# Kernel optimization log

Hardware: AMD Instinct MI355X
Metric: run time of the kernel (lower is better)

The kernel has to match this reference:

```python
import jax, jax.numpy as jnp
from jax import lax
import numpy as np

B, T = 4096, 32
VOCAB, E, H, NCLS = 10000, 300, 300, 2


def setup_inputs() -> dict:
    key = jax.random.key(0)
    ks = jax.random.split(key, 10)
    cap = jax.random.randint(ks[0], (B, T), 0, VOCAB)
    cap_len = jax.random.randint(ks[1], (B,), 1, T + 1)  # lengths in [1, T]
    embed_w = jax.random.uniform(ks[2], (VOCAB, E), jnp.float32, -0.1, 0.1)
    s = 1.0 / np.sqrt(H)
    W_ih = jax.random.uniform(ks[3], (4 * H, E), jnp.float32, -s, s)
    W_hh = jax.random.uniform(ks[4], (4 * H, H), jnp.float32, -s, s)
    b_ih = jax.random.uniform(ks[5], (4 * H,), jnp.float32, -s, s)
    b_hh = jax.random.uniform(ks[6], (4 * H,), jnp.float32, -s, s)
    cls_v = jax.random.normal(ks[7], (NCLS, H), jnp.float32) * 0.05
    cls_g = jnp.linalg.norm(cls_v, axis=1, keepdims=True)  # weight_norm init: g = ||v||
    cls_b = jax.random.uniform(ks[8], (NCLS,), jnp.float32, -s, s)
    return {"cap": cap, "cap_len": cap_len, "embed_w": embed_w,
            "W_ih": W_ih, "W_hh": W_hh, "b_ih": b_ih, "b_hh": b_hh,
            "cls_v": cls_v, "cls_g": cls_g, "cls_b": cls_b}


def _lstm_forward(cap, cap_len, embed_w, W_ih, W_hh, b_ih, b_hh, cls_v, cls_g, cls_b):
    bsz = cap.shape[0]
    hid = W_hh.shape[1]
    emb = embed_w[cap]                                   # [B, T, E]
    # Precompute the input projections for all timesteps at once (one big GEMM).
    x_gates = jnp.einsum('bte,ge->btg', emb, W_ih) + b_ih + b_hh  # [B, T, 4H]

    def step(carry, xg_t):
        h, c = carry
        gates = xg_t + h @ W_hh.T                        # [B, 4H]
        i, f, g, o = jnp.split(gates, 4, axis=-1)        # torch gate order i,f,g,o
        i = jax.nn.sigmoid(i)
        f = jax.nn.sigmoid(f)
        g = jnp.tanh(g)
        o = jax.nn.sigmoid(o)
        c = f * c + i * g
        h = o * jnp.tanh(c)
        return (h, c), h

    h0 = jnp.zeros((bsz, hid), emb.dtype)
    (_, _), hs = lax.scan(step, (h0, h0), jnp.swapaxes(x_gates, 0, 1))  # hs: [T, B, H]
    h_last = hs[cap_len - 1, jnp.arange(bsz)]            # last valid hidden state per sample
    # weight-normed classifier: W = g * v / ||v||_row  (dropout is identity in eval)
    W = cls_g * cls_v / jnp.linalg.norm(cls_v, axis=1, keepdims=True)
    return h_last @ W.T + cls_b


def reference(cap, cap_len, embed_w, W_ih, W_hh, b_ih, b_hh, cls_v, cls_g, cls_b):
    return _lstm_forward(cap, cap_len, embed_w, W_ih, W_hh, b_ih, b_hh, cls_v, cls_g, cls_b)
```

## Files before the change

kernel.cpp:

```cpp
#include <hip/hip_runtime.h>
#include <hip/hip_fp16.h>

typedef _Float16 f16;
typedef _Float16 f16x4 __attribute__((ext_vector_type(4)));
typedef _Float16 f16x8 __attribute__((ext_vector_type(8)));
typedef float f32x4 __attribute__((ext_vector_type(4)));

#define B_SZ   4096
#define T_SZ   32
#define VOCAB  10000
#define E_SZ   300
#define H_SZ   300
#define KP     320
#define GP     304
#define G4     1216
#define LDA    328
#define LDG    1224
#define LDC    308
#define ROWS   16
#define NBLK   (B_SZ/ROWS)

__device__ __forceinline__ float sigmoid_f(float x) {
    return 1.f / (1.f + __expf(-x));
}
__device__ __forceinline__ float tanh_f(float x) {
    return 2.f / (1.f + __expf(-2.f * x)) - 1.f;
}

__global__ void kP0(const float* __restrict__ ew, f16* __restrict__ embT) {
    int v = blockIdx.x, k = threadIdx.x;
    embT[(size_t)v * KP + k] = (k < E_SZ) ? (f16)ew[(size_t)v * E_SZ + k] : (f16)0.f;
}

__global__ void kPW2(const float* __restrict__ wih, const float* __restrict__ whh,
                     const float* __restrict__ bih, const float* __restrict__ bhh,
                     f16* __restrict__ Wpk, float* __restrict__ biasp) {
    int bid = blockIdx.x;
    int lane = threadIdx.x;
    int k = bid % 20, ntg = bid / 20;
    int nt = ntg % 19, gate = ntg / 19;
    int c = lane & 15, q = lane >> 4;
    int j = nt * 16 + c;
    int src = gate * H_SZ + j;
    f16 vals[8];
#pragma unroll
    for (int jj = 0; jj < 8; ++jj) {
        int kk = k * 32 + q * 8 + jj;
        float v = 0.f;
        if (j < H_SZ) {
            if (kk < KP) { if (kk < H_SZ) v = whh[(size_t)src * H_SZ + kk]; }
            else { int kx = kk - KP; if (kx < E_SZ) v = wih[(size_t)src * E_SZ + kx]; }
        }
        vals[jj] = (f16)v;
    }
    *(f16x8*)(Wpk + ((size_t)bid * 64 + lane) * 8) = *(const f16x8*)vals;
    if (k == 0 && q == 0)
        biasp[gate * GP + j] = (j < H_SZ) ? (bih[src] + bhh[src]) : 0.f;
}

__global__ void kPW4(const float* __restrict__ whh, f16* __restrict__ WgS) {
    int bid = blockIdx.x;
    int lane = threadIdx.x;
    int c = lane & 15, q = lane >> 4;
    f16 vals[8];
    if (bid < 760) {
        int nt = bid / 40, g = (bid % 40) / 10, k = bid % 10;
        int j = nt * 16 + c;
        int src = g * H_SZ + j;
#pragma unroll
        for (int jj = 0; jj < 8; ++jj) {
            int kk = k * 32 + q * 8 + jj;
            float v = (j < H_SZ && kk < H_SZ) ? whh[(size_t)src * H_SZ + kk] : 0.f;
            vals[jj] = (f16)v;
        }
    } else {
#pragma unroll
        for (int jj = 0; jj < 8; ++jj) vals[jj] = (f16)0.f;
    }
    *(f16x8*)(WgS + ((size_t)bid * 64 + lane) * 8) = *(const f16x8*)vals;
}

__global__ void kP2(const float* __restrict__ cls_v, const float* __restrict__ cls_g,
                    float* __restrict__ Wc) {
    int lane = threadIdx.x;
    for (int cl = 0; cl < 2; ++cl) {
        float s = 0.f;
        for (int j = lane; j < H_SZ; j += 64) { float v = cls_v[cl * H_SZ + j]; s += v * v; }
        for (int off = 32; off; off >>= 1) s += __shfl_down(s, off);
        float nrm = sqrtf(__shfl(s, 0));
        float scale = cls_g[cl] / nrm;
        for (int j = lane; j < GP; j += 64)
            Wc[cl * GP + j] = (j < H_SZ) ? cls_v[cl * H_SZ + j] * scale : 0.f;
    }
}

__global__ __launch_bounds__(512, 2)
void kX2(const f16* __restrict__ embT, const f16* __restrict__ Wpk,
         const float* __restrict__ biasp, f16* __restrict__ embX) {
    int tid = threadIdx.x;
    int v0 = blockIdx.x * 16;
    int wave = tid >> 6, lane = tid & 63;
    int c = lane & 15, q = lane >> 4;
    int gate = wave >> 1, half = wave & 1;
    int nt0 = half * 10, ntiles = half ? 9 : 10;
    const f16* wp0 = Wpk + (((size_t)(gate * 19 + nt0) * 20 + 10) * 64 + lane) * 8;
    f16x8 afr[10];
    const f16* arow = embT + (size_t)(v0 + c) * KP + q * 8;
#pragma unroll
    for (int k = 0; k < 10; ++k)
        afr[k] = *(const f16x8*)(arow + k * 32);
    f16x8 buf[10];
#pragma unroll
    for (int s = 0; s < 10; ++s)
        buf[s] = *(const f16x8*)(wp0 + (size_t)s * 512);
#pragma unroll 1
    for (int nt = 0; nt < ntiles - 1; ++nt) {
        int jcol = (nt0 + nt) * 16 + c;
        float bia = biasp[gate * GP + jcol];
        f32x4 acc = {bia, bia, bia, bia};
#pragma unroll
        for (int k = 0; k < 10; ++k) {
            acc = __builtin_amdgcn_mfma_f32_16x16x32_f16(afr[k], buf[k], acc, 0, 0, 0);
            buf[k] = *(const f16x8*)(wp0 + (size_t)(nt * 20 + k + 20) * 512);
        }
#pragma unroll
        for (int r = 0; r < 4; ++r)
            embX[((size_t)(v0 + q * 4 + r) * GP + jcol) * 4 + gate] = (f16)acc[r];
    }
    {
        int nt = ntiles - 1;
        int jcol = (nt0 + nt) * 16 + c;
        float bia = biasp[gate * GP + jcol];
        f32x4 acc = {bia, bia, bia, bia};
#pragma unroll
        for (int k = 0; k < 10; ++k)
            acc = __builtin_amdgcn_mfma_f32_16x16x32_f16(afr[k], buf[k], acc, 0, 0, 0);
#pragma unroll
        for (int r = 0; r < 4; ++r)
            embX[((size_t)(v0 + q * 4 + r) * GP + jcol) * 4 + gate] = (f16)acc[r];
    }
}

__global__ __launch_bounds__(512, 2)
void kR22(const int* __restrict__ cap,
          const int* __restrict__ cap_len,
          const f16* __restrict__ embX,
          const f16* __restrict__ WgS,
          const float* __restrict__ Wc,
          const float* __restrict__ cls_b,
          float* __restrict__ out) {
    extern __shared__ __align__(16) char smem[];
    f16*   hbufA = (f16*)smem;
    float* cbuf  = (float*)(smem + 20992);
    int*   capv  = (int*)(smem + 40704);
    int*   lens  = (int*)(smem + 42752);
    f16*   wres  = (f16*)(smem + 43008);
    int tid = threadIdx.x;
    int b0 = blockIdx.x * ROWS;
    if (tid < ROWS) lens[tid] = cap_len[b0 + tid];
    for (int i = tid; i < ROWS * T_SZ; i += 512) capv[i] = cap[(size_t)b0 * T_SZ + i];
    for (int i = tid; i < 2 * ROWS * LDA; i += 512) hbufA[i] = (f16)0.f;
    for (int i = tid; i < ROWS * LDC; i += 512) cbuf[i] = 0.f;

    int wave = tid >> 6, lane = tid & 63;
    int c = lane & 15, q = lane >> 4;
    int tstart = (wave < 5) ? 2 * wave : 10 + 3 * (wave - 5);
    int tcnt   = (wave < 5) ? 2 : 3;
    int Rw     = (wave < 5) ? 1 : 2;
    f16* resw = wres + ((wave < 5) ? wave * 5120 : 25600 + (wave - 5) * 10240);
    for (int u = 0; u < Rw; ++u)
#pragma unroll
        for (int k = 0; k < 10; ++k)
            *(f16x8*)(resw + (u * 10 + k) * 512 + lane * 8) =
                *(const f16x8*)(WgS + ((size_t)(tstart * 40 + u * 10 + k) * 64 + lane) * 8);
    __syncthreads();

    const f16* wp0 = WgS + ((size_t)(tstart * 40) * 64 + lane) * 8;
    int cur = 0;
    f16x8 buf[10];
#pragma unroll
    for (int s = 0; s < 10; ++s)
        buf[s] = *(const f16x8*)(wp0 + (size_t)(Rw * 10 + s) * 512);

    for (int t = 0; t < T_SZ; ++t) {
        const f16* hb = hbufA + cur * (ROWS * LDA);
        f16*       hn = hbufA + (cur ^ 1) * (ROWS * LDA);
        f16x8 afr[10];
#pragma unroll
        for (int k = 0; k < 10; ++k)
            afr[k] = *(const f16x8*)(hb + c * LDA + k * 32 + q * 8);
#pragma unroll 1
        for (int nt = 0; nt < tcnt; ++nt) {
            int col = (tstart + nt) * 16 + c;
            f16x4 xi[4];
#pragma unroll
            for (int r = 0; r < 4; ++r) {
                int v = capv[(q * 4 + r) * T_SZ + t];
                xi[r] = *(const f16x4*)(embX + (size_t)v * G4 + col * 4);
            }
            f32x4 acc0 = {0.f, 0.f, 0.f, 0.f};
            f32x4 acc1 = {0.f, 0.f, 0.f, 0.f};
            f32x4 acc2 = {0.f, 0.f, 0.f, 0.f};
            f32x4 acc3 = {0.f, 0.f, 0.f, 0.f};
#pragma unroll
            for (int g = 0; g < 4; ++g) {
                f32x4* ag = (g == 0) ? &acc0 : (g == 1) ? &acc1 : (g == 2) ? &acc2 : &acc3;
                if (nt == 0 && g < Rw) {
                    const f16* rb = resw + g * 5120 + lane * 8;
#pragma unroll
                    for (int k = 0; k < 10; ++k)
                        *ag = __builtin_amdgcn_mfma_f32_16x16x32_f16(
                            afr[k], *(const f16x8*)(rb + k * 512), *ag, 0, 0, 0);
                } else {
                    int nbase = (g < 3) ? (nt * 40 + (g + 1) * 10)
                              : ((nt + 1 < tcnt) ? (nt + 1) * 40 : Rw * 10);
#pragma unroll
                    for (int k = 0; k < 10; ++k) {
                        *ag = __builtin_amdgcn_mfma_f32_16x16x32_f16(
                            afr[k], buf[k], *ag, 0, 0, 0);
                        buf[k] = *(const f16x8*)(wp0 + (size_t)(nbase + k) * 512);
                    }
                }
            }
#pragma unroll
            for (int r = 0; r < 4; ++r) {
                int row = q * 4 + r;
                f16x4 xv = xi[r];
                float gi = acc0[r] + (float)xv[0];
                float gf = acc1[r] + (float)xv[1];
                float gg = acc2[r] + (float)xv[2];
                float go = acc3[r] + (float)xv[3];
                float ii = sigmoid_f(gi);
                float ff = sigmoid_f(gf);
                float gt = tanh_f(gg);
                float oo = sigmoid_f(go);
                int ci = row * LDC + col;
                float cn = ff * cbuf[ci] + ii * gt;
                cbuf[ci] = cn;
                float hh = oo * tanh_f(cn);
                hn[row * LDA + col] = (f16)hh;
                if (t == lens[row] - 1) {
                    float s0 = hh * Wc[col];
                    float s1 = hh * Wc[GP + col];
                    s0 += __shfl_xor(s0, 1); s1 += __shfl_xor(s1, 1);
                    s0 += __shfl_xor(s0, 2); s1 += __shfl_xor(s1, 2);
                    s0 += __shfl_xor(s0, 4); s1 += __shfl_xor(s1, 4);
                    s0 += __shfl_xor(s0, 8); s1 += __shfl_xor(s1, 8);
                    if (c == 0) {
                        if (wave == 0 && nt == 0) { s0 += cls_b[0]; s1 += cls_b[1]; }
                        atomicAdd(out + (size_t)(b0 + row) * 2 + 0, s0);
                        atomicAdd(out + (size_t)(b0 + row) * 2 + 1, s1);
                    }
                }
            }
        }
        __syncthreads();
        cur ^= 1;
    }
}

__global__ __launch_bounds__(512, 2)
void kR8(const int* __restrict__ cap,
         const int* __restrict__ cap_len,
         const f16* __restrict__ embT,
         const f16* __restrict__ Wpk,
         const float* __restrict__ biasp,
         float* __restrict__ hlast) {
    extern __shared__ __align__(16) char smem[];
    f16*   hbuf  = (f16*)smem;
    f16*   xbuf  = (f16*)(smem + 10496);
    f16*   gates = (f16*)(smem + 20992);
    float* biasL = (float*)(smem + 60160);
    int*   capv  = (int*)(smem + 65024);
    int*   lens  = (int*)(smem + 67072);
    int tid = threadIdx.x;
    int b0 = blockIdx.x * 16;
    if (tid < 16) lens[tid] = cap_len[b0 + tid];
    for (int i = tid; i < 16 * T_SZ; i += 512) capv[i] = cap[(size_t)b0 * T_SZ + i];
    for (int i = tid; i < 16 * LDA; i += 512) hbuf[i] = (f16)0.f;
    for (int i = tid; i < G4; i += 512) biasL[i] = biasp[i];
    __syncthreads();
    for (int i = tid; i < 16 * 40; i += 512) {
        int m = i / 40, c8 = i - m * 40;
        int v = capv[m * T_SZ + 0];
        *(f16x8*)(xbuf + m * LDA + c8 * 8) = *(const f16x8*)(embT + (size_t)v * KP + c8 * 8);
    }
    __syncthreads();
    int wave = tid >> 6, lane = tid & 63;
    int c = lane & 15, q = lane >> 4;
    int gate = wave >> 1, half = wave & 1;
    int nt0 = half * 10, ntiles = half ? 9 : 10;
    const f16* wp0 = Wpk + ((size_t)((gate * 19 + nt0) * 20) * 64 + lane) * 8;
    const f16* hrow = hbuf + c * LDA + q * 8;
    const f16* xrow = xbuf + c * LDA + q * 8;
    float creg[10];
#pragma unroll
    for (int i = 0; i < 10; ++i) creg[i] = 0.f;

    for (int t = 0; t < T_SZ; ++t) {
        f16x8 afr[10];
#pragma unroll
        for (int k = 0; k < 10; ++k)
            afr[k] = *(const f16x8*)(hrow + k * 32);
        f16x8 buf[10];
#pragma unroll
        for (int s = 0; s < 10; ++s)
            buf[s] = *(const f16x8*)(wp0 + (size_t)s * 512);
#pragma unroll 1
        for (int nt = 0; nt < ntiles - 1; ++nt) {
            int base = nt * 20;
            int ncol = gate * GP + (nt0 + nt) * 16 + c;
            float bia = biasL[ncol];
            f32x4 acch = {bia, bia, bia, bia};
            f32x4 accx = {0.f, 0.f, 0.f, 0.f};
#pragma unroll
            for (int k = 0; k < 20; ++k) {
                if (k < 10) {
                    acch = __builtin_amdgcn_mfma_f32_16x16x32_f16(afr[k], buf[k % 10], acch, 0, 0, 0);
                } else {
                    f16x8 a = *(const f16x8*)(xrow + (k - 10) * 32);
                    accx = __builtin_amdgcn_mfma_f32_16x16x32_f16(a, buf[k % 10], accx, 0, 0, 0);
                }
                buf[k % 10] = *(const f16x8*)(wp0 + (size_t)(base + k + 10) * 512);
            }
#pragma unroll
            for (int r = 0; r < 4; ++r)
                gates[(q * 4 + r) * LDG + ncol] = (f16)(acch[r] + accx[r]);
        }
        {
            int nt = ntiles - 1;
            int base = nt * 20;
            int ncol = gate * GP + (nt0 + nt) * 16 + c;
            float bia = biasL[ncol];
            f32x4 acch = {bia, bia, bia, bia};
            f32x4 accx = {0.f, 0.f, 0.f, 0.f};
#pragma unroll
            for (int k = 0; k < 20; ++k) {
                if (k < 10) {
                    acch = __builtin_amdgcn_mfma_f32_16x16x32_f16(afr[k], buf[k % 10], acch, 0, 0, 0);
                    buf[k % 10] = *(const f16x8*)(wp0 + (size_t)(base + k + 10) * 512);
                } else {
                    f16x8 a = *(const f16x8*)(xrow + (k - 10) * 32);
                    accx = __builtin_amdgcn_mfma_f32_16x16x32_f16(a, buf[k % 10], accx, 0, 0, 0);
                }
            }
#pragma unroll
            for (int r = 0; r < 4; ++r)
                gates[(q * 4 + r) * LDG + ncol] = (f16)(acch[r] + accx[r]);
        }
        __syncthreads();
        int tp1 = t + 1;
        if (tp1 < T_SZ) {
            for (int i = tid; i < 16 * 40; i += 512) {
                int m = i / 40, c8 = i - m * 40;
                int v = capv[m * T_SZ + tp1];
                *(f16x8*)(xbuf + m * LDA + c8 * 8) =
                    *(const f16x8*)(embT + (size_t)v * KP + c8 * 8);
            }
        }
#pragma unroll
        for (int it = 0; it < 10; ++it) {
            int idx = tid + it * 512;
            int m = idx / 320, j = idx - m * 320;
            if (j < H_SZ) {
                const f16* gr = gates + m * LDG;
                float gi = (float)gr[j];
                float gf = (float)gr[GP + j];
                float gg = (float)gr[2 * GP + j];
                float go = (float)gr[3 * GP + j];
                float ii = sigmoid_f(gi);
                float ff = sigmoid_f(gf);
                float gt = tanh_f(gg);
                float oo = sigmoid_f(go);
                float cn = ff * creg[it] + ii * gt;
                creg[it] = cn;
                float hh = oo * tanh_f(cn);
                hbuf[m * LDA + j] = (f16)hh;
                if (t == lens[m] - 1) hlast[(size_t)(b0 + m) * GP + j] = hh;
            }
        }
        __syncthreads();
    }
}

__global__ void kC(const float* __restrict__ hlast, const float* __restrict__ Wc,
                   const float* __restrict__ cls_b, float* __restrict__ out) {
    int row = blockIdx.x, lane = threadIdx.x;
    const float* h = hlast + (size_t)row * GP;
    float s0 = 0.f, s1 = 0.f;
    for (int j = lane; j < H_SZ; j += 64) {
        float hv = h[j];
        s0 += hv * Wc[j];
        s1 += hv * Wc[GP + j];
    }
    for (int off = 32; off; off >>= 1) {
        s0 += __shfl_down(s0, off);
        s1 += __shfl_down(s1, off);
    }
    if (lane == 0) {
        out[row * 2 + 0] = s0 + cls_b[0];
        out[row * 2 + 1] = s1 + cls_b[1];
    }
}

extern "C" void kernel_launch(void* const* d_in, const int* in_sizes, int n_in,
                              void* d_out, int out_size, void* d_ws, size_t ws_size,
                              hipStream_t stream) {
    const int*   cap     = (const int*)d_in[0];
    const int*   cap_len = (const int*)d_in[1];
    const float* embed_w = (const float*)d_in[2];
    const float* W_ih    = (const float*)d_in[3];
    const float* W_hh    = (const float*)d_in[4];
    const float* b_ih    = (const float*)d_in[5];
    const float* b_hh    = (const float*)d_in[6];
    const float* cls_v   = (const float*)d_in[7];
    const float* cls_g   = (const float*)d_in[8];
    const float* cls_b   = (const float*)d_in[9];
    float* out = (float*)d_out;

    char* w = (char*)d_ws;
    size_t off = 0;
    auto alloc = [&](size_t bytes) -> void* {
        void* p = w + off;
        off += (bytes + 255) & ~(size_t)255;
        return p;
    };
    f16*   embT  = (f16*)alloc((size_t)VOCAB * KP * sizeof(f16));
    f16*   Wpk   = (f16*)alloc((size_t)1520 * 64 * 8 * sizeof(f16));
    f16*   WgS   = (f16*)alloc((size_t)800 * 64 * 8 * sizeof(f16));
    float* biasp = (float*)alloc((size_t)G4 * sizeof(float));
    float* Wc    = (float*)alloc((size_t)2 * GP * sizeof(float));
    float* hlast = (float*)alloc((size_t)B_SZ * GP * sizeof(float));
    f16*   embX  = (f16*)(w + off);
    size_t need_split = off + ((size_t)VOCAB * GP * 4 * sizeof(f16) + 255);
    bool split = (ws_size >= need_split);

    kP0<<<VOCAB, KP, 0, stream>>>(embed_w, embT);
    kPW2<<<1520, 64, 0, stream>>>(W_ih, W_hh, b_ih, b_hh, Wpk, biasp);
    kP2<<<1, 64, 0, stream>>>(cls_v, cls_g, Wc);
    if (split) {
        (void)hipMemsetAsync(out, 0, (size_t)out_size, stream);
        kPW4<<<800, 64, 0, stream>>>(W_hh, WgS);
        kX2<<<VOCAB / 16, 512, 0, stream>>>(embT, Wpk, biasp, embX);
        static const int smem_r22 = 155648;
        (void)hipFuncSetAttribute((const void*)kR22,
                                  hipFuncAttributeMaxDynamicSharedMemorySize, smem_r22);
        kR22<<<NBLK, 512, smem_r22, stream>>>(cap, cap_len, embX, WgS, Wc, cls_b, out);
    } else {
        static const int smem_r8 = 67072 + 64;
        (void)hipFuncSetAttribute((const void*)kR8,
                                  hipFuncAttributeMaxDynamicSharedMemorySize, smem_r8);
        kR8<<<B_SZ / 16, 512, smem_r8, stream>>>(cap, cap_len, embT, Wpk, biasp, hlast);
        kC<<<B_SZ, 64, 0, stream>>>(hlast, Wc, cls_b, out);
    }
}
```

Measured before the change: 409.4 us.

## Rebalance W_hh residency: waves 0-4 keep two gate slices in LDS, double-buffer streams

Restructures the recurrent kernel's weight schedule. Waves 0-4 now keep two gate slices of W_hh resident in LDS, while waves 5-7 keep none and stream all weights through two register buffers (bufA/bufB) with explicit per-gate prefetch offsets. The A fragments from h are now reloaded from LDS for each MFMA instead of being held in registers, and the per-timestep tile loop is unrolled into explicit straight-line code. This trades more LDS reads per step and a smaller total LDS footprint for lower register pressure and better latency hiding of the streamed weight loads.

```diff
diff --git a/kernel.cpp b/kernel.cpp
--- a/kernel.cpp
+++ b/kernel.cpp
@@ -142,7 +142,7 @@
 }
 
 __global__ __launch_bounds__(512, 2)
-void kR22(const int* __restrict__ cap,
+void kR24(const int* __restrict__ cap,
           const int* __restrict__ cap_len,
           const f16* __restrict__ embX,
           const f16* __restrict__ WgS,
@@ -154,7 +154,7 @@
     float* cbuf  = (float*)(smem + 20992);
     int*   capv  = (int*)(smem + 40704);
     int*   lens  = (int*)(smem + 42752);
-    f16*   wres  = (f16*)(smem + 43008);
+    f16*   wres  = (f16*)(smem + 42816);
     int tid = threadIdx.x;
     int b0 = blockIdx.x * ROWS;
     if (tid < ROWS) lens[tid] = cap_len[b0 + tid];
@@ -165,71 +165,75 @@
     int wave = tid >> 6, lane = tid & 63;
     int c = lane & 15, q = lane >> 4;
     int tstart = (wave < 5) ? 2 * wave : 10 + 3 * (wave - 5);
-    int tcnt   = (wave < 5) ? 2 : 3;
-    int Rw     = (wave < 5) ? 1 : 2;
-    f16* resw = wres + ((wave < 5) ? wave * 5120 : 25600 + (wave - 5) * 10240);
-    for (int u = 0; u < Rw; ++u)
-#pragma unroll
-        for (int k = 0; k < 10; ++k)
-            *(f16x8*)(resw + (u * 10 + k) * 512 + lane * 8) =
-                *(const f16x8*)(WgS + ((size_t)(tstart * 40 + u * 10 + k) * 64 + lane) * 8);
+    const f16* wp0 = WgS + ((size_t)(tstart * 40) * 64 + lane) * 8;
+    f16* resw = wres + wave * 20480;
+    if (wave < 5) {
+#pragma unroll
+        for (int u = 0; u < 2; ++u)
+#pragma unroll
+            for (int k = 0; k < 10; ++k)
+                *(f16x8*)(resw + (u * 10 + k) * 512 + lane * 8) =
+                    *(const f16x8*)(WgS + ((size_t)(tstart * 40 + u * 10 + k) * 64 + lane) * 8);
+    }
     __syncthreads();
 
-    const f16* wp0 = WgS + ((size_t)(tstart * 40) * 64 + lane) * 8;
+    f16x8 bufA[10], bufB[10];
+    if (wave < 5) {
+#pragma unroll
+        for (int k = 0; k < 10; ++k) {
+            bufA[k] = *(const f16x8*)(wp0 + (size_t)(20 + k) * 512);
+            bufB[k] = *(const f16x8*)(wp0 + (size_t)(30 + k) * 512);
+        }
+    } else {
+#pragma unroll
+        for (int k = 0; k < 10; ++k) {
+            bufA[k] = *(const f16x8*)(wp0 + (size_t)(0 + k) * 512);
+            bufB[k] = *(const f16x8*)(wp0 + (size_t)(10 + k) * 512);
+        }
+    }
     int cur = 0;
-    f16x8 buf[10];
-#pragma unroll
-    for (int s = 0; s < 10; ++s)
-        buf[s] = *(const f16x8*)(wp0 + (size_t)(Rw * 10 + s) * 512);
-
+
+#pragma unroll 1
     for (int t = 0; t < T_SZ; ++t) {
         const f16* hb = hbufA + cur * (ROWS * LDA);
         f16*       hn = hbufA + (cur ^ 1) * (ROWS * LDA);
-        f16x8 afr[10];
-#pragma unroll
-        for (int k = 0; k < 10; ++k)
-            afr[k] = *(const f16x8*)(hb + c * LDA + k * 32 + q * 8);
-#pragma unroll 1
-        for (int nt = 0; nt < tcnt; ++nt) {
+        const f16* ab = hb + c * LDA + q * 8;
+        f16x4 xi[4];
+
+        auto SU = [&](f32x4& acc, f16x8* BUF, int pf) {
+#pragma unroll
+            for (int k = 0; k < 10; ++k) {
+                f16x8 af = *(const f16x8*)(ab + k * 32);
+                acc = __builtin_amdgcn_mfma_f32_16x16x32_f16(af, BUF[k], acc, 0, 0, 0);
+                BUF[k] = *(const f16x8*)(wp0 + (size_t)(pf + k) * 512);
+            }
+        };
+        auto RU = [&](f32x4& acc, int u) {
+#pragma unroll
+            for (int k = 0; k < 10; ++k) {
+                f16x8 af = *(const f16x8*)(ab + k * 32);
+                f16x8 wv = *(const f16x8*)(resw + (u * 10 + k) * 512 + lane * 8);
+                acc = __builtin_amdgcn_mfma_f32_16x16x32_f16(af, wv, acc, 0, 0, 0);
+            }
+        };
+        auto XG = [&](int nt) {
             int col = (tstart + nt) * 16 + c;
-            f16x4 xi[4];
 #pragma unroll
             for (int r = 0; r < 4; ++r) {
                 int v = capv[(q * 4 + r) * T_SZ + t];
                 xi[r] = *(const f16x4*)(embX + (size_t)v * G4 + col * 4);
             }
-            f32x4 acc0 = {0.f, 0.f, 0.f, 0.f};
-            f32x4 acc1 = {0.f, 0.f, 0.f, 0.f};
-            f32x4 acc2 = {0.f, 0.f, 0.f, 0.f};
-            f32x4 acc3 = {0.f, 0.f, 0.f, 0.f};
-#pragma unroll
-            for (int g = 0; g < 4; ++g) {
-                f32x4* ag = (g == 0) ? &acc0 : (g == 1) ? &acc1 : (g == 2) ? &acc2 : &acc3;
-                if (nt == 0 && g < Rw) {
-                    const f16* rb = resw + g * 5120 + lane * 8;
-#pragma unroll
-                    for (int k = 0; k < 10; ++k)
-                        *ag = __builtin_amdgcn_mfma_f32_16x16x32_f16(
-                            afr[k], *(const f16x8*)(rb + k * 512), *ag, 0, 0, 0);
-                } else {
-                    int nbase = (g < 3) ? (nt * 40 + (g + 1) * 10)
-                              : ((nt + 1 < tcnt) ? (nt + 1) * 40 : Rw * 10);
-#pragma unroll
-                    for (int k = 0; k < 10; ++k) {
-                        *ag = __builtin_amdgcn_mfma_f32_16x16x32_f16(
-                            afr[k], buf[k], *ag, 0, 0, 0);
-                        buf[k] = *(const f16x8*)(wp0 + (size_t)(nbase + k) * 512);
-                    }
-                }
-            }
+        };
+        auto CELL = [&](int nt, f32x4& a0, f32x4& a1, f32x4& a2, f32x4& a3) {
+            int col = (tstart + nt) * 16 + c;
 #pragma unroll
             for (int r = 0; r < 4; ++r) {
                 int row = q * 4 + r;
                 f16x4 xv = xi[r];
-                float gi = acc0[r] + (float)xv[0];
-                float gf = acc1[r] + (float)xv[1];
-                float gg = acc2[r] + (float)xv[2];
-                float go = acc3[r] + (float)xv[3];
+                float gi = a0[r] + (float)xv[0];
+                float gf = a1[r] + (float)xv[1];
+                float gg = a2[r] + (float)xv[2];
+                float go = a3[r] + (float)xv[3];
                 float ii = sigmoid_f(gi);
                 float ff = sigmoid_f(gf);
                 float gt = tanh_f(gg);
@@ -253,6 +257,50 @@
                     }
                 }
             }
+        };
+
+        if (wave < 5) {
+            f32x4 a0 = {0.f,0.f,0.f,0.f}, a1 = {0.f,0.f,0.f,0.f};
+            f32x4 a2 = {0.f,0.f,0.f,0.f}, a3 = {0.f,0.f,0.f,0.f};
+            XG(0);
+            RU(a0, 0);
+            RU(a1, 1);
+            SU(a2, bufA, 40);
+            SU(a3, bufB, 50);
+            CELL(0, a0, a1, a2, a3);
+            a0 = (f32x4){0.f,0.f,0.f,0.f}; a1 = (f32x4){0.f,0.f,0.f,0.f};
+            a2 = (f32x4){0.f,0.f,0.f,0.f}; a3 = (f32x4){0.f,0.f,0.f,0.f};
+            XG(1);
+            SU(a0, bufA, 60);
+            SU(a1, bufB, 70);
+            SU(a2, bufA, 20);
+            SU(a3, bufB, 30);
+            CELL(1, a0, a1, a2, a3);
+        } else {
+            f32x4 a0 = {0.f,0.f,0.f,0.f}, a1 = {0.f,0.f,0.f,0.f};
+            f32x4 a2 = {0.f,0.f,0.f,0.f}, a3 = {0.f,0.f,0.f,0.f};
+            XG(0);
+            SU(a0, bufA, 20);
+            SU(a1, bufB, 30);
+            SU(a2, bufA, 40);
+            SU(a3, bufB, 50);
+            CELL(0, a0, a1, a2, a3);
+            a0 = (f32x4){0.f,0.f,0.f,0.f}; a1 = (f32x4){0.f,0.f,0.f,0.f};
+            a2 = (f32x4){0.f,0.f,0.f,0.f}; a3 = (f32x4){0.f,0.f,0.f,0.f};
+            XG(1);
+            SU(a0, bufA, 60);
+            SU(a1, bufB, 70);
+            SU(a2, bufA, 80);
+            SU(a3, bufB, 90);
+            CELL(1, a0, a1, a2, a3);
+            a0 = (f32x4){0.f,0.f,0.f,0.f}; a1 = (f32x4){0.f,0.f,0.f,0.f};
+            a2 = (f32x4){0.f,0.f,0.f,0.f}; a3 = (f32x4){0.f,0.f,0.f,0.f};
+            XG(2);
+            SU(a0, bufA, 100);
+            SU(a1, bufB, 110);
+            SU(a2, bufA, 0);
+            SU(a3, bufB, 10);
+            CELL(2, a0, a1, a2, a3);
         }
         __syncthreads();
         cur ^= 1;
@@ -442,10 +490,10 @@
         (void)hipMemsetAsync(out, 0, (size_t)out_size, stream);
         kPW4<<<800, 64, 0, stream>>>(W_hh, WgS);
         kX2<<<VOCAB / 16, 512, 0, stream>>>(embT, Wpk, biasp, embX);
-        static const int smem_r22 = 155648;
-        (void)hipFuncSetAttribute((const void*)kR22,
-                                  hipFuncAttributeMaxDynamicSharedMemorySize, smem_r22);
-        kR22<<<NBLK, 512, smem_r22, stream>>>(cap, cap_len, embX, WgS, Wc, cls_b, out);
+        static const int smem_r24 = 145216;
+        (void)hipFuncSetAttribute((const void*)kR24,
+                                  hipFuncAttributeMaxDynamicSharedMemorySize, smem_r24);
+        kR24<<<NBLK, 512, smem_r24, stream>>>(cap, cap_len, embX, WgS, Wc, cls_b, out);
     } else {
         static const int smem_r8 = 67072 + 64;
         (void)hipFuncSetAttribute((const void*)kR8,
```

Result: slower. 1.003 ms (+144.9%).

## Rebalance LSTM recurrence weight residency and use a deeper register prefetch ring

Applied to the files above, without the earlier changes.

The recurrent kernel changes how W_hh slices are split between shared memory and registers. The five 2-tile waves now keep two gate slices resident in LDS, while the three 3-tile waves stream all their weights through a 15-entry register ring instead of a 10-entry buffer, so loads are issued further ahead. The loops are fully unrolled through macros, and the A fragments are read from LDS per MFMA instead of being held in registers. This aims to hide global weight-load latency and free registers, at the cost of extra LDS reads and register pressure from the larger ring, which could affect occupancy at 2 blocks per CU.

```diff
diff --git a/kernel.cpp b/kernel.cpp
--- a/kernel.cpp
+++ b/kernel.cpp
@@ -141,8 +141,66 @@
     }
 }
 
+#define ZACC() do { a0 = (f32x4){0.f,0.f,0.f,0.f}; a1 = (f32x4){0.f,0.f,0.f,0.f}; \
+                    a2 = (f32x4){0.f,0.f,0.f,0.f}; a3 = (f32x4){0.f,0.f,0.f,0.f}; } while (0)
+#define SU(ACC, U, BASE, MOD) do { \
+    _Pragma("unroll") \
+    for (int k = 0; k < 10; ++k) { \
+        f16x8 af_ = *(const f16x8*)(ab + k * 32); \
+        ACC = __builtin_amdgcn_mfma_f32_16x16x32_f16(af_, ring[((U) * 10 + k) % 15], ACC, 0, 0, 0); \
+        ring[((U) * 10 + k) % 15] = \
+            *(const f16x8*)(wp0 + (size_t)((BASE) + (((U) * 10 + k + 15) % (MOD))) * 512); \
+    } } while (0)
+#define RU(ACC, UU) do { \
+    _Pragma("unroll") \
+    for (int k = 0; k < 10; ++k) { \
+        f16x8 af_ = *(const f16x8*)(ab + k * 32); \
+        f16x8 wv_ = *(const f16x8*)(resw + ((UU) * 10 + k) * 512 + lane * 8); \
+        ACC = __builtin_amdgcn_mfma_f32_16x16x32_f16(af_, wv_, ACC, 0, 0, 0); \
+    } } while (0)
+#define XG(NT) do { \
+    int col_ = (tstart + (NT)) * 16 + c; \
+    _Pragma("unroll") \
+    for (int r = 0; r < 4; ++r) { \
+        int v_ = capv[(q * 4 + r) * T_SZ + t]; \
+        xi[r] = *(const f16x4*)(embX + (size_t)v_ * G4 + col_ * 4); \
+    } } while (0)
+#define CELL(NT) do { \
+    int col_ = (tstart + (NT)) * 16 + c; \
+    _Pragma("unroll") \
+    for (int r = 0; r < 4; ++r) { \
+        int row_ = q * 4 + r; \
+        f16x4 xv_ = xi[r]; \
+        float gi = a0[r] + (float)xv_[0]; \
+        float gf = a1[r] + (float)xv_[1]; \
+        float gg = a2[r] + (float)xv_[2]; \
+        float go = a3[r] + (float)xv_[3]; \
+        float ii = sigmoid_f(gi); \
+        float ff = sigmoid_f(gf); \
+        float gt = tanh_f(gg); \
+        float oo = sigmoid_f(go); \
+        int ci_ = row_ * LDC + col_; \
+        float cn = ff * cbuf[ci_] + ii * gt; \
+        cbuf[ci_] = cn; \
+        float hh = oo * tanh_f(cn); \
+        hn[row_ * LDA + col_] = (f16)hh; \
+        if (t == lens[row_] - 1) { \
+            float s0 = hh * Wc[col_]; \
+            float s1 = hh * Wc[GP + col_]; \
+            s0 += __shfl_xor(s0, 1); s1 += __shfl_xor(s1, 1); \
+            s0 += __shfl_xor(s0, 2); s1 += __shfl_xor(s1, 2); \
+            s0 += __shfl_xor(s0, 4); s1 += __shfl_xor(s1, 4); \
+            s0 += __shfl_xor(s0, 8); s1 += __shfl_xor(s1, 8); \
+            if (c == 0) { \
+                if (wave == 0 && (NT) == 0) { s0 += cls_b[0]; s1 += cls_b[1]; } \
+                atomicAdd(out + (size_t)(b0 + row_) * 2 + 0, s0); \
+                atomicAdd(out + (size_t)(b0 + row_) * 2 + 1, s1); \
+            } \
+        } \
+    } } while (0)
+
 __global__ __launch_bounds__(512, 2)
-void kR22(const int* __restrict__ cap,
+void kR25(const int* __restrict__ cap,
           const int* __restrict__ cap_len,
           const f16* __restrict__ embX,
           const f16* __restrict__ WgS,
@@ -154,7 +212,7 @@
     float* cbuf  = (float*)(smem + 20992);
     int*   capv  = (int*)(smem + 40704);
     int*   lens  = (int*)(smem + 42752);
-    f16*   wres  = (f16*)(smem + 43008);
+    f16*   wres  = (f16*)(smem + 42816);
     int tid = threadIdx.x;
     int b0 = blockIdx.x * ROWS;
     if (tid < ROWS) lens[tid] = cap_len[b0 + tid];
@@ -165,94 +223,56 @@
     int wave = tid >> 6, lane = tid & 63;
     int c = lane & 15, q = lane >> 4;
     int tstart = (wave < 5) ? 2 * wave : 10 + 3 * (wave - 5);
-    int tcnt   = (wave < 5) ? 2 : 3;
-    int Rw     = (wave < 5) ? 1 : 2;
-    f16* resw = wres + ((wave < 5) ? wave * 5120 : 25600 + (wave - 5) * 10240);
-    for (int u = 0; u < Rw; ++u)
-#pragma unroll
-        for (int k = 0; k < 10; ++k)
-            *(f16x8*)(resw + (u * 10 + k) * 512 + lane * 8) =
-                *(const f16x8*)(WgS + ((size_t)(tstart * 40 + u * 10 + k) * 64 + lane) * 8);
+    const f16* wp0 = WgS + ((size_t)(tstart * 40) * 64 + lane) * 8;
+    f16* resw = wres + wave * 20480;
+    if (wave < 5) {
+#pragma unroll
+        for (int u = 0; u < 2; ++u)
+#pragma unroll
+            for (int k = 0; k < 10; ++k)
+                *(f16x8*)(resw + (u * 10 + k) * 512 + lane * 8) =
+                    *(const f16x8*)(wp0 + (size_t)(u * 10 + k) * 512);
+    }
     __syncthreads();
 
-    const f16* wp0 = WgS + ((size_t)(tstart * 40) * 64 + lane) * 8;
+    f16x8 ring[15];
+    {
+        int base = (wave < 5) ? 20 : 0;
+#pragma unroll
+        for (int s = 0; s < 15; ++s)
+            ring[s] = *(const f16x8*)(wp0 + (size_t)(base + s) * 512);
+    }
     int cur = 0;
-    f16x8 buf[10];
-#pragma unroll
-    for (int s = 0; s < 10; ++s)
-        buf[s] = *(const f16x8*)(wp0 + (size_t)(Rw * 10 + s) * 512);
-
+
+#pragma unroll 1
     for (int t = 0; t < T_SZ; ++t) {
         const f16* hb = hbufA + cur * (ROWS * LDA);
         f16*       hn = hbufA + (cur ^ 1) * (ROWS * LDA);
-        f16x8 afr[10];
-#pragma unroll
-        for (int k = 0; k < 10; ++k)
-            afr[k] = *(const f16x8*)(hb + c * LDA + k * 32 + q * 8);
-#pragma unroll 1
-        for (int nt = 0; nt < tcnt; ++nt) {
-            int col = (tstart + nt) * 16 + c;
-            f16x4 xi[4];
-#pragma unroll
-            for (int r = 0; r < 4; ++r) {
-                int v = capv[(q * 4 + r) * T_SZ + t];
-                xi[r] = *(const f16x4*)(embX + (size_t)v * G4 + col * 4);
-            }
-            f32x4 acc0 = {0.f, 0.f, 0.f, 0.f};
-            f32x4 acc1 = {0.f, 0.f, 0.f, 0.f};
-            f32x4 acc2 = {0.f, 0.f, 0.f, 0.f};
-            f32x4 acc3 = {0.f, 0.f, 0.f, 0.f};
-#pragma unroll
-            for (int g = 0; g < 4; ++g) {
-                f32x4* ag = (g == 0) ? &acc0 : (g == 1) ? &acc1 : (g == 2) ? &acc2 : &acc3;
-                if (nt == 0 && g < Rw) {
-                    const f16* rb = resw + g * 5120 + lane * 8;
-#pragma unroll
-                    for (int k = 0; k < 10; ++k)
-                        *ag = __builtin_amdgcn_mfma_f32_16x16x32_f16(
-                            afr[k], *(const f16x8*)(rb + k * 512), *ag, 0, 0, 0);
-                } else {
-                    int nbase = (g < 3) ? (nt * 40 + (g + 1) * 10)
-                              : ((nt + 1 < tcnt) ? (nt + 1) * 40 : Rw * 10);
-#pragma unroll
-                    for (int k = 0; k < 10; ++k) {
-                        *ag = __builtin_amdgcn_mfma_f32_16x16x32_f16(
-                            afr[k], buf[k], *ag, 0, 0, 0);
-                        buf[k] = *(const f16x8*)(wp0 + (size_t)(nbase + k) * 512);
-                    }
-                }
-            }
-#pragma unroll
-            for (int r = 0; r < 4; ++r) {
-                int row = q * 4 + r;
-                f16x4 xv = xi[r];
-                float gi = acc0[r] + (float)xv[0];
-                float gf = acc1[r] + (float)xv[1];
-                float gg = acc2[r] + (float)xv[2];
-                float go = acc3[r] + (float)xv[3];
-                float ii = sigmoid_f(gi);
-                float ff = sigmoid_f(gf);
-                float gt = tanh_f(gg);
-                float oo = sigmoid_f(go);
-                int ci = row * LDC + col;
-                float cn = ff * cbuf[ci] + ii * gt;
-                cbuf[ci] = cn;
-                float hh = oo * tanh_f(cn);
-                hn[row * LDA + col] = (f16)hh;
-                if (t == lens[row] - 1) {
-                    float s0 = hh * Wc[col];
-                    float s1 = hh * Wc[GP + col];
-                    s0 += __shfl_xor(s0, 1); s1 += __shfl_xor(s1, 1);
-                    s0 += __shfl_xor(s0, 2); s1 += __shfl_xor(s1, 2);
-                    s0 += __shfl_xor(s0, 4); s1 += __shfl_xor(s1, 4);
-                    s0 += __shfl_xor(s0, 8); s1 += __shfl_xor(s1, 8);
-                    if (c == 0) {
-                        if (wave == 0 && nt == 0) { s0 += cls_b[0]; s1 += cls_b[1]; }
-                        atomicAdd(out + (size_t)(b0 + row) * 2 + 0, s0);
-                        atomicAdd(out + (size_t)(b0 + row) * 2 + 1, s1);
-                    }
-                }
-            }
+        const f16* ab = hb + c * LDA + q * 8;
+        f16x4 xi[4];
+        f32x4 a0, a1, a2, a3;
+        if (wave < 5) {
+            XG(0); ZACC();
+            RU(a0, 0); RU(a1, 1);
+            SU(a2, 0, 20, 60); SU(a3, 1, 20, 60);
+            CELL(0);
+            XG(1); ZACC();
+            SU(a0, 2, 20, 60); SU(a1, 3, 20, 60);
+            SU(a2, 4, 20, 60); SU(a3, 5, 20, 60);
+            CELL(1);
+        } else {
+            XG(0); ZACC();
+            SU(a0, 0, 0, 120); SU(a1, 1, 0, 120);
+            SU(a2, 2, 0, 120); SU(a3, 3, 0, 120);
+            CELL(0);
+            XG(1); ZACC();
+            SU(a0, 4, 0, 120); SU(a1, 5, 0, 120);
+            SU(a2, 6, 0, 120); SU(a3, 7, 0, 120);
+            CELL(1);
+            XG(2); ZACC();
+            SU(a0, 8, 0, 120); SU(a1, 9, 0, 120);
+            SU(a2, 10, 0, 120); SU(a3, 11, 0, 120);
+            CELL(2);
         }
         __syncthreads();
         cur ^= 1;
@@ -442,10 +462,10 @@
         (void)hipMemsetAsync(out, 0, (size_t)out_size, stream);
         kPW4<<<800, 64, 0, stream>>>(W_hh, WgS);
         kX2<<<VOCAB / 16, 512, 0, stream>>>(embT, Wpk, biasp, embX);
-        static const int smem_r22 = 155648;
-        (void)hipFuncSetAttribute((const void*)kR22,
-                                  hipFuncAttributeMaxDynamicSharedMemorySize, smem_r22);
-        kR22<<<NBLK, 512, smem_r22, stream>>>(cap, cap_len, embX, WgS, Wc, cls_b, out);
+        static const int smem_r25 = 145216;
+        (void)hipFuncSetAttribute((const void*)kR25,
+                                  hipFuncAttributeMaxDynamicSharedMemorySize, smem_r25);
+        kR25<<<NBLK, 512, smem_r25, stream>>>(cap, cap_len, embX, WgS, Wc, cls_b, out);
     } else {
         static const int smem_r8 = 67072 + 64;
         (void)hipFuncSetAttribute((const void*)kR8,
```

Result: slower. 807.5 us (+97.2%).
